# Kernel tuning notes

Measured on AMD Instinct MI355X. Metric: run time of the kernel, lower is better.

The kernel has to match this reference:

```python
import jax, jax.numpy as jnp
import numpy as np

N = 100000      # total nodes (batched graphs)
E = 1200000     # total edges
A = 256         # annotation size (hidden_size_orig)
H = 64          # gnn_h_size
T = 4           # num_edge_types
STEPS = 6       # num_timesteps
B = 64          # number of graphs in the batch
NUM_CLS = 2


def setup_inputs() -> dict:
    key = jax.random.key(0)
    ks = jax.random.split(key, 16)
    annotation = jax.random.normal(ks[0], (N, A), dtype=jnp.float32)
    src = jax.random.randint(ks[1], (E,), 0, N, dtype=jnp.int32)
    dst = jax.random.randint(ks[2], (E,), 0, N, dtype=jnp.int32)
    etypes = jax.random.randint(ks[3], (E,), 0, T, dtype=jnp.int32)
    graph_ids = jnp.sort(jax.random.randint(ks[4], (N,), 0, B, dtype=jnp.int32))

    def lin(k, fan_in, shape):
        return jax.random.normal(k, shape, dtype=jnp.float32) / np.sqrt(fan_in).astype(np.float32)

    params = {
        'reduce_W': lin(ks[5], A, (A, H)),
        'reduce_b': jnp.zeros((H,), jnp.float32),
        'edge_W': lin(ks[6], H, (T, H, H)),      # per-edge-type linear
        'edge_b': jnp.zeros((T, H), jnp.float32),
        'gru_Wi': lin(ks[7], H, (3 * H, H)),     # torch GRUCell layout: r,z,n
        'gru_bi': jnp.zeros((3 * H,), jnp.float32),
        'gru_Wh': lin(ks[8], H, (3 * H, H)),
        'gru_bh': jnp.zeros((3 * H,), jnp.float32),
        'gate_W': lin(ks[9], 2 * H, (2 * H, 1)),
        'gate_b': jnp.zeros((1,), jnp.float32),
        'out_W': lin(ks[10], 2 * H, (2 * H, NUM_CLS)),
        'out_b': jnp.zeros((NUM_CLS,), jnp.float32),
    }
    return dict(annotation=annotation, src=src, dst=dst, etypes=etypes,
                graph_ids=graph_ids, **params)


def reference(annotation, src, dst, etypes, graph_ids,
              reduce_W, reduce_b, edge_W, edge_b,
              gru_Wi, gru_bi, gru_Wh, gru_bh,
              gate_W, gate_b, out_W, out_b):
    # reduce_layer
    h0 = annotation @ reduce_W + reduce_b            # [N, H]

    def step(h, _):
        # per-edge-type linear on all nodes: [T, N, H]
        transformed = jnp.einsum('nh,thk->tnk', h, edge_W) + edge_b[:, None, :]
        msg = transformed[etypes, src]               # [E, H] gather per edge
        a = jax.ops.segment_sum(msg, dst, num_segments=N)  # scatter-add
        # GRUCell(a, h)
        gi = a @ gru_Wi.T + gru_bi
        gh = h @ gru_Wh.T + gru_bh
        i_r, i_z, i_n = jnp.split(gi, 3, axis=-1)
        h_r, h_z, h_n = jnp.split(gh, 3, axis=-1)
        r = jax.nn.sigmoid(i_r + h_r)
        z = jax.nn.sigmoid(i_z + h_z)
        n = jnp.tanh(i_n + r * h_n)
        h_new = (1.0 - z) * n + z * h
        return h_new, None

    h, _ = jax.lax.scan(step, h0, None, length=STEPS)

    feat = jnp.concatenate([h, h0], axis=-1)         # [N, 2H]

    # GlobalAttentionPooling: segment softmax over gate scores, weighted sum
    gate = feat @ gate_W + gate_b                    # [N, 1]
    gmax = jax.ops.segment_max(gate, graph_ids, num_segments=B)
    gmax = jnp.where(jnp.isfinite(gmax), gmax, 0.0)  # guard empty graphs
    e = jnp.exp(gate - gmax[graph_ids])
    denom = jax.ops.segment_sum(e, graph_ids, num_segments=B)
    alpha = e / denom[graph_ids]                     # [N, 1]
    readout = jax.ops.segment_sum(alpha * feat, graph_ids, num_segments=B)  # [B, 2H]

    logits = readout @ out_W + out_b                 # [B, 2]
    return logits
```

## Files before the change

kernel.cpp:

```cpp
#include <hip/hip_runtime.h>
#include <cstdint>
#include <cstddef>

#define N_NODES 100000
#define N_EDGES 1200000
#define ASIZE 256
#define HSIZE 64
#define NTYPES 4
#define NSTEPS 6
#define NGRAPH 64
#define PS 16

static __device__ __forceinline__ float sigmoidf_(float x) { return 1.0f / (1.0f + expf(-x)); }

__global__ void k_count(const int* __restrict__ dst, int* __restrict__ deg) {
    int e = blockIdx.x * 256 + threadIdx.x;
    if (e < N_EDGES) atomicAdd(&deg[dst[e]], 1);
}

__global__ void k_scan1(const int* __restrict__ deg, int* __restrict__ rs, int* __restrict__ part) {
    __shared__ int sh[256];
    int t = threadIdx.x;
    int base = blockIdx.x * 1024 + t * 4;
    int v0 = (base + 0 < N_NODES) ? deg[base + 0] : 0;
    int v1 = (base + 1 < N_NODES) ? deg[base + 1] : 0;
    int v2 = (base + 2 < N_NODES) ? deg[base + 2] : 0;
    int v3 = (base + 3 < N_NODES) ? deg[base + 3] : 0;
    int s = v0 + v1 + v2 + v3;
    sh[t] = s;
    __syncthreads();
    for (int off = 1; off < 256; off <<= 1) {
        int x = (t >= off) ? sh[t - off] : 0;
        __syncthreads();
        sh[t] += x;
        __syncthreads();
    }
    int excl = sh[t] - s;
    if (t == 255) part[blockIdx.x] = sh[255];
    if (base + 0 < N_NODES) rs[base + 0] = excl;
    if (base + 1 < N_NODES) rs[base + 1] = excl + v0;
    if (base + 2 < N_NODES) rs[base + 2] = excl + v0 + v1;
    if (base + 3 < N_NODES) rs[base + 3] = excl + v0 + v1 + v2;
}

__global__ void k_scan2(int* __restrict__ part, int* __restrict__ rs, int nb) {
    if (threadIdx.x == 0 && blockIdx.x == 0) {
        int run = 0;
        for (int i = 0; i < nb; ++i) { int v = part[i]; part[i] = run; run += v; }
        rs[N_NODES] = run;
    }
}

__global__ void k_scan3(int* __restrict__ rs, const int* __restrict__ part) {
    int i = blockIdx.x * 256 + threadIdx.x;
    if (i < N_NODES) rs[i] += part[i >> 10];
}

__global__ void k_fill(const int* __restrict__ src, const int* __restrict__ dst,
                       const int* __restrict__ ety, const int* __restrict__ rs,
                       int* __restrict__ cur, int* __restrict__ colidx) {
    int e = blockIdx.x * 256 + threadIdx.x;
    if (e < N_EDGES) {
        int d = dst[e];
        int pos = rs[d] + atomicAdd(&cur[d], 1);
        colidx[pos] = src[e] * 448 + 192 + ety[e] * 64;
    }
}

__global__ void k_prep2(const float* __restrict__ Wh, const float* __restrict__ Bh,
                        const float* __restrict__ eW, const float* __restrict__ eb,
                        const float* __restrict__ Wi, const float* __restrict__ Bi,
                        float* __restrict__ W448, float* __restrict__ bias448,
                        float* __restrict__ WiA, float* __restrict__ biA) {
    int idx = blockIdx.x * 256 + threadIdx.x;
    if (idx < 64 * 448) {
        int k = idx / 448, m = idx % 448;
        float v;
        if (m < 192) {
            int j = m / 3, g = m % 3;
            v = Wh[(g * 64 + j) * 64 + k];
        } else {
            v = eW[(size_t)(m - 192 >> 6) * 4096 + k * 64 + ((m - 192) & 63)];
        }
        W448[idx] = v;
    }
    if (idx < 64 * 192) {
        int k = idx / 192, m = idx % 192;
        int j = m / 3, g = m % 3;
        WiA[idx] = Wi[(g * 64 + j) * 64 + k];
    }
    if (idx < 448) {
        bias448[idx] = (idx < 192) ? Bh[(idx % 3) * 64 + idx / 3] : eb[idx - 192];
    }
    if (idx < 192) {
        biA[idx] = Bi[(idx % 3) * 64 + idx / 3];
    }
}

__global__ __launch_bounds__(256) void k_gemm(const float* __restrict__ X, int ldx, int K,
                                              const float* __restrict__ W, int ldw,
                                              const float* __restrict__ bias,
                                              float* __restrict__ Y, float* __restrict__ Y2,
                                              int M) {
    __shared__ float sX[128 * 66];
    __shared__ float sW[64 * 64];
    int tid = threadIdx.x;
    int mtile = blockIdx.x * 64;
    int ntile = blockIdx.y * 128;
    int tc4 = (tid & 15) * 4;
    int tr = tid >> 4;
    float4 acc[8];
#pragma unroll
    for (int i = 0; i < 8; ++i) acc[i] = make_float4(0.f, 0.f, 0.f, 0.f);

    int nkc = K >> 6;
    for (int kc = 0; kc < nkc; ++kc) {
        if (kc) __syncthreads();
#pragma unroll
        for (int i = 0; i < 8; ++i) {
            int lin4 = (i * 256 + tid) * 4;
            int nl = lin4 >> 6, kk = lin4 & 63;
            int n = ntile + nl;
            float4 v = make_float4(0.f, 0.f, 0.f, 0.f);
            if (n < N_NODES) v = *(const float4*)(X + (size_t)n * ldx + kc * 64 + kk);
            float* d = sX + nl * 66 + kk;
            d[0] = v.x; d[1] = v.y; d[2] = v.z; d[3] = v.w;
        }
#pragma unroll
        for (int i = 0; i < 4; ++i) {
            int lin4 = (i * 256 + tid) * 4;
            int kk = lin4 >> 6, c = lin4 & 63;
            float4 v = *(const float4*)(W + (size_t)(kc * 64 + kk) * ldw + mtile + c);
            *(float4*)(sW + kk * 64 + c) = v;
        }
        __syncthreads();
        const float* xr = sX + tr * 8 * 66;
        const float* wr = sW + tc4;
        for (int kk = 0; kk < 64; kk += 2) {
            float4 wA = *(const float4*)(wr + kk * 64);
            float4 wB = *(const float4*)(wr + (kk + 1) * 64);
            float xA[8], xB[8];
#pragma unroll
            for (int i = 0; i < 8; ++i) { xA[i] = xr[i * 66 + kk]; xB[i] = xr[i * 66 + kk + 1]; }
#pragma unroll
            for (int i = 0; i < 8; ++i) {
                acc[i].x = fmaf(xA[i], wA.x, acc[i].x);
                acc[i].y = fmaf(xA[i], wA.y, acc[i].y);
                acc[i].z = fmaf(xA[i], wA.z, acc[i].z);
                acc[i].w = fmaf(xA[i], wA.w, acc[i].w);
            }
#pragma unroll
            for (int i = 0; i < 8; ++i) {
                acc[i].x = fmaf(xB[i], wB.x, acc[i].x);
                acc[i].y = fmaf(xB[i], wB.y, acc[i].y);
                acc[i].z = fmaf(xB[i], wB.z, acc[i].z);
                acc[i].w = fmaf(xB[i], wB.w, acc[i].w);
            }
        }
    }
    float4 bv = *(const float4*)(bias + mtile + tc4);
#pragma unroll
    for (int i = 0; i < 8; ++i) {
        int n = ntile + tr * 8 + i;
        if (n < N_NODES) {
            float4 y;
            y.x = acc[i].x + bv.x; y.y = acc[i].y + bv.y;
            y.z = acc[i].z + bv.z; y.w = acc[i].w + bv.w;
            *(float4*)(Y + (size_t)n * M + mtile + tc4) = y;
            if (Y2) *(float4*)(Y2 + (size_t)n * M + mtile + tc4) = y;
        }
    }
}

__global__ void k_aggregate(const float* __restrict__ buf1, const int* __restrict__ rs,
                            const int* __restrict__ colidx, float* __restrict__ a) {
    int l = threadIdx.x & 63;
    int n = blockIdx.x * 4 + (threadIdx.x >> 6);
    int beg = rs[n], end = rs[n + 1];
    float a0 = 0.f, a1 = 0.f, a2 = 0.f, a3 = 0.f;
    int s = beg;
    for (; s + 3 < end; s += 4) {
        int c0 = colidx[s], c1 = colidx[s + 1], c2 = colidx[s + 2], c3 = colidx[s + 3];
        a0 += buf1[(size_t)c0 + l];
        a1 += buf1[(size_t)c1 + l];
        a2 += buf1[(size_t)c2 + l];
        a3 += buf1[(size_t)c3 + l];
    }
    for (; s < end; ++s) a0 += buf1[(size_t)colidx[s] + l];
    a[(size_t)n * 64 + l] = (a0 + a1) + (a2 + a3);
}

__global__ __launch_bounds__(256) void k_gruF(const float* __restrict__ A,
                                              const float* __restrict__ WiA,
                                              const float* __restrict__ biA,
                                              const float* __restrict__ buf1,
                                              float* __restrict__ H) {
    __shared__ float sX[64 * 34];
    __shared__ float sW[32 * 192];
    int tid = threadIdx.x;
    int ntile = blockIdx.x * 64;
    int tc = tid & 15;
    int tr = tid >> 4;
    float acc[4][12];
#pragma unroll
    for (int i = 0; i < 4; ++i)
#pragma unroll
        for (int c = 0; c < 12; ++c) acc[i][c] = 0.f;

    for (int kc = 0; kc < 2; ++kc) {
        if (kc) __syncthreads();
#pragma unroll
        for (int i = 0; i < 2; ++i) {
            int lin4 = (i * 256 + tid) * 4;
            int nl = lin4 >> 5, kk = lin4 & 31;
            int n = ntile + nl;
            float4 v = make_float4(0.f, 0.f, 0.f, 0.f);
            if (n < N_NODES) v = *(const float4*)(A + (size_t)n * 64 + kc * 32 + kk);
            float* d = sX + nl * 34 + kk;
            d[0] = v.x; d[1] = v.y; d[2] = v.z; d[3] = v.w;
        }
        {
            int kk = tid >> 3, c = (tid & 7) * 24;
            const float* srcp = WiA + (size_t)(kc * 32 + kk) * 192 + c;
            float* d = sW + kk * 192 + c;
#pragma unroll
            for (int u = 0; u < 6; ++u) *(float4*)(d + 4 * u) = *(const float4*)(srcp + 4 * u);
        }
        __syncthreads();
        const float* xr = sX + tr * 4 * 34;
        const float* wr = sW + tc * 12;
        for (int kk = 0; kk < 32; kk += 2) {
            float4 w0 = *(const float4*)(wr + kk * 192);
            float4 w1 = *(const float4*)(wr + kk * 192 + 4);
            float4 w2 = *(const float4*)(wr + kk * 192 + 8);
            float4 u0 = *(const float4*)(wr + (kk + 1) * 192);
            float4 u1 = *(const float4*)(wr + (kk + 1) * 192 + 4);
            float4 u2 = *(const float4*)(wr + (kk + 1) * 192 + 8);
            float xA[4], xB[4];
#pragma unroll
            for (int i = 0; i < 4; ++i) { xA[i] = xr[i * 34 + kk]; xB[i] = xr[i * 34 + kk + 1]; }
#pragma unroll
            for (int i = 0; i < 4; ++i) {
                acc[i][0]  = fmaf(xA[i], w0.x, acc[i][0]);
                acc[i][1]  = fmaf(xA[i], w0.y, acc[i][1]);
                acc[i][2]  = fmaf(xA[i], w0.z, acc[i][2]);
                acc[i][3]  = fmaf(xA[i], w0.w, acc[i][3]);
                acc[i][4]  = fmaf(xA[i], w1.x, acc[i][4]);
                acc[i][5]  = fmaf(xA[i], w1.y, acc[i][5]);
                acc[i][6]  = fmaf(xA[i], w1.z, acc[i][6]);
                acc[i][7]  = fmaf(xA[i], w1.w, acc[i][7]);
                acc[i][8]  = fmaf(xA[i], w2.x, acc[i][8]);
                acc[i][9]  = fmaf(xA[i], w2.y, acc[i][9]);
                acc[i][10] = fmaf(xA[i], w2.z, acc[i][10]);
                acc[i][11] = fmaf(xA[i], w2.w, acc[i][11]);
            }
#pragma unroll
            for (int i = 0; i < 4; ++i) {
                acc[i][0]  = fmaf(xB[i], u0.x, acc[i][0]);
                acc[i][1]  = fmaf(xB[i], u0.y, acc[i][1]);
                acc[i][2]  = fmaf(xB[i], u0.z, acc[i][2]);
                acc[i][3]  = fmaf(xB[i], u0.w, acc[i][3]);
                acc[i][4]  = fmaf(xB[i], u1.x, acc[i][4]);
                acc[i][5]  = fmaf(xB[i], u1.y, acc[i][5]);
                acc[i][6]  = fmaf(xB[i], u1.z, acc[i][6]);
                acc[i][7]  = fmaf(xB[i], u1.w, acc[i][7]);
                acc[i][8]  = fmaf(xB[i], u2.x, acc[i][8]);
                acc[i][9]  = fmaf(xB[i], u2.y, acc[i][9]);
                acc[i][10] = fmaf(xB[i], u2.z, acc[i][10]);
                acc[i][11] = fmaf(xB[i], u2.w, acc[i][11]);
            }
        }
    }
    float bb[12];
    {
        float4 b0 = *(const float4*)(biA + tc * 12);
        float4 b1 = *(const float4*)(biA + tc * 12 + 4);
        float4 b2 = *(const float4*)(biA + tc * 12 + 8);
        bb[0] = b0.x; bb[1] = b0.y; bb[2] = b0.z; bb[3] = b0.w;
        bb[4] = b1.x; bb[5] = b1.y; bb[6] = b1.z; bb[7] = b1.w;
        bb[8] = b2.x; bb[9] = b2.y; bb[10] = b2.z; bb[11] = b2.w;
    }
#pragma unroll
    for (int i = 0; i < 4; ++i) {
        int n = ntile + tr * 4 + i;
        if (n >= N_NODES) continue;
        const float* ghp = buf1 + (size_t)n * 448 + tc * 12;
        float gg[12];
        float4 g0 = *(const float4*)(ghp);
        float4 g1 = *(const float4*)(ghp + 4);
        float4 g2 = *(const float4*)(ghp + 8);
        gg[0] = g0.x; gg[1] = g0.y; gg[2] = g0.z; gg[3] = g0.w;
        gg[4] = g1.x; gg[5] = g1.y; gg[6] = g1.z; gg[7] = g1.w;
        gg[8] = g2.x; gg[9] = g2.y; gg[10] = g2.z; gg[11] = g2.w;
        float4 hv = *(const float4*)(H + (size_t)n * 64 + tc * 4);
        float res[4];
#pragma unroll
        for (int jj = 0; jj < 4; ++jj) {
            int c = jj * 3;
            float r = sigmoidf_(acc[i][c] + bb[c] + gg[c]);
            float z = sigmoidf_(acc[i][c + 1] + bb[c + 1] + gg[c + 1]);
            float nn = tanhf(acc[i][c + 2] + bb[c + 2] + r * gg[c + 2]);
            float hj = (jj == 0) ? hv.x : (jj == 1) ? hv.y : (jj == 2) ? hv.z : hv.w;
            res[jj] = (1.f - z) * nn + z * hj;
        }
        float4 o; o.x = res[0]; o.y = res[1]; o.z = res[2]; o.w = res[3];
        *(float4*)(H + (size_t)n * 64 + tc * 4) = o;
    }
}

__global__ void k_bounds(const int* __restrict__ gid, int* __restrict__ start) {
    int n = blockIdx.x * 256 + threadIdx.x;
    if (n < N_NODES) {
        int g = gid[n];
        if (n == 0) {
            for (int x = 0; x <= g; ++x) start[x] = 0;
        } else {
            int pg = gid[n - 1];
            for (int x = pg + 1; x <= g; ++x) start[x] = n;
        }
        if (n == N_NODES - 1) {
            for (int x = g + 1; x <= NGRAPH; ++x) start[x] = N_NODES;
        }
    }
}

__global__ void k_gate2(const float* __restrict__ H, const float* __restrict__ H0,
                        const float* __restrict__ gW, const float* __restrict__ gb,
                        float* __restrict__ gate) {
    int l = threadIdx.x & 63;
    int n = blockIdx.x * 4 + (threadIdx.x >> 6);
    float v = H[(size_t)n * 64 + l] * gW[l] + H0[(size_t)n * 64 + l] * gW[64 + l];
    for (int off = 32; off > 0; off >>= 1) v += __shfl_xor(v, off, 64);
    if (l == 0) gate[n] = v + gb[0];
}

__global__ __launch_bounds__(64) void k_poolA(const float* __restrict__ gate,
                                              const int* __restrict__ start,
                                              float* __restrict__ pmax) {
    int g = blockIdx.x, s = blockIdx.y;
    int beg = start[g], len = start[g + 1] - beg;
    int sb = beg + (int)((long long)len * s / PS);
    int se = beg + (int)((long long)len * (s + 1) / PS);
    float m = -INFINITY;
    for (int n = sb + threadIdx.x; n < se; n += 64) m = fmaxf(m, gate[n]);
    for (int off = 32; off > 0; off >>= 1) m = fmaxf(m, __shfl_xor(m, off, 64));
    if (threadIdx.x == 0) pmax[g * PS + s] = m;
}

__global__ void k_poolB(const float* __restrict__ pmax, float* __restrict__ gm) {
    int g = threadIdx.x;
    float m = -INFINITY;
    for (int s = 0; s < PS; ++s) m = fmaxf(m, pmax[g * PS + s]);
    if (!isfinite(m)) m = 0.0f;
    gm[g] = m;
}

__global__ __launch_bounds__(256) void k_poolC(const float* __restrict__ H,
                                               const float* __restrict__ H0,
                                               const float* __restrict__ gate,
                                               const int* __restrict__ start,
                                               const float* __restrict__ gm,
                                               float* __restrict__ pnum,
                                               float* __restrict__ pden) {
    int g = blockIdx.x, s = blockIdx.y;
    int beg = start[g], len = start[g + 1] - beg;
    int sb = beg + (int)((long long)len * s / PS);
    int se = beg + (int)((long long)len * (s + 1) / PS);
    int t = threadIdx.x;
    int lane = t & 63, wave = t >> 6;
    float m = gm[g];
    __shared__ float shh[4][64], sh0[4][64], ses[4];
    float ah = 0.f, ah0 = 0.f, es = 0.f;
    for (int n = sb + wave; n < se; n += 4) {
        float e = expf(gate[n] - m);
        es += e;
        ah  += e * H [(size_t)n * 64 + lane];
        ah0 += e * H0[(size_t)n * 64 + lane];
    }
    shh[wave][lane] = ah; sh0[wave][lane] = ah0;
    if (lane == 0) ses[wave] = es;
    __syncthreads();
    if (wave == 0) {
        float r  = shh[0][lane] + shh[1][lane] + shh[2][lane] + shh[3][lane];
        float r0 = sh0[0][lane] + sh0[1][lane] + sh0[2][lane] + sh0[3][lane];
        int base = (g * PS + s) * 128;
        pnum[base + lane]      = r;
        pnum[base + 64 + lane] = r0;
        if (lane == 0) pden[g * PS + s] = ses[0] + ses[1] + ses[2] + ses[3];
    }
}

__global__ __launch_bounds__(128) void k_poolD(const float* __restrict__ pnum,
                                               const float* __restrict__ pden,
                                               float* __restrict__ ro) {
    int g = blockIdx.x;
    int c = threadIdx.x;
    float den = 0.f;
    for (int s = 0; s < PS; ++s) den += pden[g * PS + s];
    float nu = 0.f;
    for (int s = 0; s < PS; ++s) nu += pnum[(g * PS + s) * 128 + c];
    ro[g * 128 + c] = (den > 0.f) ? nu / den : 0.f;
}

__global__ void k_logits(const float* __restrict__ ro, const float* __restrict__ oW,
                         const float* __restrict__ ob, float* __restrict__ out) {
    int t = threadIdx.x;
    int b = t >> 1;
    int c = t & 1;
    float acc = ob[c];
    for (int k = 0; k < 128; ++k) acc = fmaf(ro[b * 128 + k], oW[k * 2 + c], acc);
    out[b * 2 + c] = acc;
}

extern "C" void kernel_launch(void* const* d_in, const int* in_sizes, int n_in,
                              void* d_out, int out_size, void* d_ws, size_t ws_size,
                              hipStream_t stream) {
    (void)in_sizes; (void)n_in; (void)out_size; (void)ws_size;
    const float* ann = (const float*)d_in[0];
    const int* src   = (const int*)d_in[1];
    const int* dst   = (const int*)d_in[2];
    const int* ety   = (const int*)d_in[3];
    const int* gid   = (const int*)d_in[4];
    const float* rW  = (const float*)d_in[5];
    const float* rb  = (const float*)d_in[6];
    const float* eW  = (const float*)d_in[7];
    const float* eb  = (const float*)d_in[8];
    const float* Wi  = (const float*)d_in[9];
    const float* Bi  = (const float*)d_in[10];
    const float* Wh  = (const float*)d_in[11];
    const float* Bh  = (const float*)d_in[12];
    const float* gW  = (const float*)d_in[13];
    const float* gb  = (const float*)d_in[14];
    const float* oW  = (const float*)d_in[15];
    const float* ob  = (const float*)d_in[16];
    float* out = (float*)d_out;

    char* p = (char*)d_ws;
    auto take = [&](size_t nbytes) -> void* {
        void* r = (void*)p;
        p += (nbytes + 255) & ~((size_t)255);
        return r;
    };
    float* h0      = (float*)take((size_t)N_NODES * 64 * 4);
    float* h       = (float*)take((size_t)N_NODES * 64 * 4);
    float* abuf    = (float*)take((size_t)N_NODES * 64 * 4);
    float* buf1    = (float*)take((size_t)N_NODES * 448 * 4);
    float* W448    = (float*)take(64 * 448 * 4);
    float* bias448 = (float*)take(448 * 4);
    float* WiA     = (float*)take(64 * 192 * 4);
    float* biA     = (float*)take(192 * 4);
    int* deg       = (int*)take((size_t)N_NODES * 4);
    int* cur       = (int*)take((size_t)N_NODES * 4);
    int* rs        = (int*)take((size_t)(N_NODES + 1) * 4);
    int* part      = (int*)take(512);
    int* colidx    = (int*)take((size_t)N_EDGES * 4);
    float* gate    = (float*)take((size_t)N_NODES * 4);
    int* start     = (int*)take((size_t)(NGRAPH + 1) * 4);
    float* pmax    = (float*)take(NGRAPH * PS * 4);
    float* gm      = (float*)take(NGRAPH * 4);
    float* pnum    = (float*)take((size_t)NGRAPH * PS * 128 * 4);
    float* pden    = (float*)take(NGRAPH * PS * 4);
    float* ro      = (float*)take(NGRAPH * 128 * 4);

    hipMemsetAsync(deg, 0, (size_t)N_NODES * 4, stream);
    hipMemsetAsync(cur, 0, (size_t)N_NODES * 4, stream);
    k_count<<<(N_EDGES + 255) / 256, 256, 0, stream>>>(dst, deg);
    int nb = (N_NODES + 1023) / 1024;
    k_scan1<<<nb, 256, 0, stream>>>(deg, rs, part);
    k_scan2<<<1, 64, 0, stream>>>(part, rs, nb);
    k_scan3<<<(N_NODES + 255) / 256, 256, 0, stream>>>(rs, part);
    k_fill<<<(N_EDGES + 255) / 256, 256, 0, stream>>>(src, dst, ety, rs, cur, colidx);

    k_prep2<<<112, 256, 0, stream>>>(Wh, Bh, eW, eb, Wi, Bi, W448, bias448, WiA, biA);
    k_bounds<<<(N_NODES + 255) / 256, 256, 0, stream>>>(gid, start);

    int ntiles = (N_NODES + 127) / 128;

    k_gemm<<<dim3(1, ntiles), 256, 0, stream>>>(ann, ASIZE, ASIZE, rW, 64, rb, h, h0, 64);

    for (int s = 0; s < NSTEPS; ++s) {
        k_gemm<<<dim3(7, ntiles), 256, 0, stream>>>(h, 64, 64, W448, 448, bias448,
                                                    buf1, nullptr, 448);
        k_aggregate<<<N_NODES / 4, 256, 0, stream>>>(buf1, rs, colidx, abuf);
        k_gruF<<<(N_NODES + 63) / 64, 256, 0, stream>>>(abuf, WiA, biA, buf1, h);
    }

    k_gate2<<<N_NODES / 4, 256, 0, stream>>>(h, h0, gW, gb, gate);
    k_poolA<<<dim3(NGRAPH, PS), 64, 0, stream>>>(gate, start, pmax);
    k_poolB<<<1, 64, 0, stream>>>(pmax, gm);
    k_poolC<<<dim3(NGRAPH, PS), 256, 0, stream>>>(h, h0, gate, start, gm, pnum, pden);
    k_poolD<<<NGRAPH, 128, 0, stream>>>(pnum, pden, ro);
    k_logits<<<1, 128, 0, stream>>>(ro, oW, ob, out);
}
```

Before: 1.588 ms.

## Specialize GEMMs: reuse X tile across all output columns, prefetch weights

```diff
diff --git a/kernel.cpp b/kernel.cpp
--- a/kernel.cpp
+++ b/kernel.cpp
@@ -97,48 +97,52 @@
     }
 }
 
-__global__ __launch_bounds__(256) void k_gemm(const float* __restrict__ X, int ldx, int K,
-                                              const float* __restrict__ W, int ldw,
-                                              const float* __restrict__ bias,
-                                              float* __restrict__ Y, float* __restrict__ Y2,
-                                              int M) {
+__global__ __launch_bounds__(256) void k_gemm_step(const float* __restrict__ X,
+                                                   const float* __restrict__ W,
+                                                   const float* __restrict__ bias,
+                                                   float* __restrict__ Y) {
     __shared__ float sX[128 * 66];
     __shared__ float sW[64 * 64];
     int tid = threadIdx.x;
-    int mtile = blockIdx.x * 64;
-    int ntile = blockIdx.y * 128;
+    int ntile = blockIdx.x * 128;
     int tc4 = (tid & 15) * 4;
     int tr = tid >> 4;
-    float4 acc[8];
-#pragma unroll
-    for (int i = 0; i < 8; ++i) acc[i] = make_float4(0.f, 0.f, 0.f, 0.f);
-
-    int nkc = K >> 6;
-    for (int kc = 0; kc < nkc; ++kc) {
-        if (kc) __syncthreads();
-#pragma unroll
-        for (int i = 0; i < 8; ++i) {
-            int lin4 = (i * 256 + tid) * 4;
-            int nl = lin4 >> 6, kk = lin4 & 63;
-            int n = ntile + nl;
-            float4 v = make_float4(0.f, 0.f, 0.f, 0.f);
-            if (n < N_NODES) v = *(const float4*)(X + (size_t)n * ldx + kc * 64 + kk);
-            float* d = sX + nl * 66 + kk;
-            d[0] = v.x; d[1] = v.y; d[2] = v.z; d[3] = v.w;
-        }
-#pragma unroll
-        for (int i = 0; i < 4; ++i) {
-            int lin4 = (i * 256 + tid) * 4;
-            int kk = lin4 >> 6, c = lin4 & 63;
-            float4 v = *(const float4*)(W + (size_t)(kc * 64 + kk) * ldw + mtile + c);
-            *(float4*)(sW + kk * 64 + c) = v;
-        }
-        __syncthreads();
-        const float* xr = sX + tr * 8 * 66;
-        const float* wr = sW + tc4;
+    int swr = tid >> 4;
+    int swc = (tid & 15) * 4;
+
+#pragma unroll
+    for (int i = 0; i < 8; ++i) {
+        int lin4 = (i * 256 + tid) * 4;
+        int nl = lin4 >> 6, kk = lin4 & 63;
+        int n = ntile + nl;
+        float4 v = make_float4(0.f, 0.f, 0.f, 0.f);
+        if (n < N_NODES) v = *(const float4*)(X + (size_t)n * 64 + kk);
+        float* d = sX + nl * 66 + kk;
+        d[0] = v.x; d[1] = v.y; d[2] = v.z; d[3] = v.w;
+    }
+    float4 wreg[4];
+#pragma unroll
+    for (int i = 0; i < 4; ++i)
+        wreg[i] = *(const float4*)(W + (size_t)(i * 16 + swr) * 448 + swc);
+#pragma unroll
+    for (int i = 0; i < 4; ++i)
+        *(float4*)(sW + (i * 16 + swr) * 64 + swc) = wreg[i];
+    __syncthreads();
+
+    const float* xr = sX + tr * 8 * 66;
+    const float* wrp = sW + tc4;
+    for (int m = 0; m < 7; ++m) {
+        if (m < 6) {
+#pragma unroll
+            for (int i = 0; i < 4; ++i)
+                wreg[i] = *(const float4*)(W + (size_t)(i * 16 + swr) * 448 + (m + 1) * 64 + swc);
+        }
+        float4 acc[8];
+#pragma unroll
+        for (int i = 0; i < 8; ++i) acc[i] = make_float4(0.f, 0.f, 0.f, 0.f);
         for (int kk = 0; kk < 64; kk += 2) {
-            float4 wA = *(const float4*)(wr + kk * 64);
-            float4 wB = *(const float4*)(wr + (kk + 1) * 64);
+            float4 wA = *(const float4*)(wrp + kk * 64);
+            float4 wB = *(const float4*)(wrp + (kk + 1) * 64);
             float xA[8], xB[8];
 #pragma unroll
             for (int i = 0; i < 8; ++i) { xA[i] = xr[i * 66 + kk]; xB[i] = xr[i * 66 + kk + 1]; }
@@ -157,8 +161,112 @@
                 acc[i].w = fmaf(xB[i], wB.w, acc[i].w);
             }
         }
-    }
-    float4 bv = *(const float4*)(bias + mtile + tc4);
+        float4 bv = *(const float4*)(bias + m * 64 + tc4);
+        if (m < 6) {
+            __syncthreads();
+#pragma unroll
+            for (int i = 0; i < 4; ++i)
+                *(float4*)(sW + (i * 16 + swr) * 64 + swc) = wreg[i];
+            __syncthreads();
+        }
+#pragma unroll
+        for (int i = 0; i < 8; ++i) {
+            int n = ntile + tr * 8 + i;
+            if (n < N_NODES) {
+                float4 y;
+                y.x = acc[i].x + bv.x; y.y = acc[i].y + bv.y;
+                y.z = acc[i].z + bv.z; y.w = acc[i].w + bv.w;
+                *(float4*)(Y + (size_t)n * 448 + m * 64 + tc4) = y;
+            }
+        }
+    }
+}
+
+__global__ __launch_bounds__(256) void k_gemm_red(const float* __restrict__ X,
+                                                  const float* __restrict__ W,
+                                                  const float* __restrict__ bias,
+                                                  float* __restrict__ Y,
+                                                  float* __restrict__ Y2) {
+    __shared__ float sX[128 * 66];
+    __shared__ float sW[64 * 64];
+    int tid = threadIdx.x;
+    int ntile = blockIdx.x * 128;
+    int tc4 = (tid & 15) * 4;
+    int tr = tid >> 4;
+    int swr = tid >> 4;
+    int swc = (tid & 15) * 4;
+
+    float4 acc[8];
+#pragma unroll
+    for (int i = 0; i < 8; ++i) acc[i] = make_float4(0.f, 0.f, 0.f, 0.f);
+
+    float4 xreg[8];
+    float4 wreg[4];
+#pragma unroll
+    for (int i = 0; i < 8; ++i) {
+        int lin4 = (i * 256 + tid) * 4;
+        int nl = lin4 >> 6, kk = lin4 & 63;
+        int n = ntile + nl;
+        float4 v = make_float4(0.f, 0.f, 0.f, 0.f);
+        if (n < N_NODES) v = *(const float4*)(X + (size_t)n * 256 + kk);
+        xreg[i] = v;
+    }
+#pragma unroll
+    for (int i = 0; i < 4; ++i)
+        wreg[i] = *(const float4*)(W + (size_t)(i * 16 + swr) * 64 + swc);
+
+    for (int kc = 0; kc < 4; ++kc) {
+#pragma unroll
+        for (int i = 0; i < 8; ++i) {
+            int lin4 = (i * 256 + tid) * 4;
+            int nl = lin4 >> 6, kk = lin4 & 63;
+            float* d = sX + nl * 66 + kk;
+            d[0] = xreg[i].x; d[1] = xreg[i].y; d[2] = xreg[i].z; d[3] = xreg[i].w;
+        }
+#pragma unroll
+        for (int i = 0; i < 4; ++i)
+            *(float4*)(sW + (i * 16 + swr) * 64 + swc) = wreg[i];
+        __syncthreads();
+        if (kc < 3) {
+#pragma unroll
+            for (int i = 0; i < 8; ++i) {
+                int lin4 = (i * 256 + tid) * 4;
+                int nl = lin4 >> 6, kk = lin4 & 63;
+                int n = ntile + nl;
+                float4 v = make_float4(0.f, 0.f, 0.f, 0.f);
+                if (n < N_NODES) v = *(const float4*)(X + (size_t)n * 256 + (kc + 1) * 64 + kk);
+                xreg[i] = v;
+            }
+#pragma unroll
+            for (int i = 0; i < 4; ++i)
+                wreg[i] = *(const float4*)(W + (size_t)((kc + 1) * 64 + i * 16 + swr) * 64 + swc);
+        }
+        const float* xr = sX + tr * 8 * 66;
+        const float* wrp = sW + tc4;
+        for (int kk = 0; kk < 64; kk += 2) {
+            float4 wA = *(const float4*)(wrp + kk * 64);
+            float4 wB = *(const float4*)(wrp + (kk + 1) * 64);
+            float xA[8], xB[8];
+#pragma unroll
+            for (int i = 0; i < 8; ++i) { xA[i] = xr[i * 66 + kk]; xB[i] = xr[i * 66 + kk + 1]; }
+#pragma unroll
+            for (int i = 0; i < 8; ++i) {
+                acc[i].x = fmaf(xA[i], wA.x, acc[i].x);
+                acc[i].y = fmaf(xA[i], wA.y, acc[i].y);
+                acc[i].z = fmaf(xA[i], wA.z, acc[i].z);
+                acc[i].w = fmaf(xA[i], wA.w, acc[i].w);
+            }
+#pragma unroll
+            for (int i = 0; i < 8; ++i) {
+                acc[i].x = fmaf(xB[i], wB.x, acc[i].x);
+                acc[i].y = fmaf(xB[i], wB.y, acc[i].y);
+                acc[i].z = fmaf(xB[i], wB.z, acc[i].z);
+                acc[i].w = fmaf(xB[i], wB.w, acc[i].w);
+            }
+        }
+        if (kc < 3) __syncthreads();
+    }
+    float4 bv = *(const float4*)(bias + tc4);
 #pragma unroll
     for (int i = 0; i < 8; ++i) {
         int n = ntile + tr * 8 + i;
@@ -166,8 +274,8 @@
             float4 y;
             y.x = acc[i].x + bv.x; y.y = acc[i].y + bv.y;
             y.z = acc[i].z + bv.z; y.w = acc[i].w + bv.w;
-            *(float4*)(Y + (size_t)n * M + mtile + tc4) = y;
-            if (Y2) *(float4*)(Y2 + (size_t)n * M + mtile + tc4) = y;
+            *(float4*)(Y + (size_t)n * 64 + tc4) = y;
+            *(float4*)(Y2 + (size_t)n * 64 + tc4) = y;
         }
     }
 }
@@ -476,11 +584,10 @@
 
     int ntiles = (N_NODES + 127) / 128;
 
-    k_gemm<<<dim3(1, ntiles), 256, 0, stream>>>(ann, ASIZE, ASIZE, rW, 64, rb, h, h0, 64);
+    k_gemm_red<<<ntiles, 256, 0, stream>>>(ann, rW, rb, h, h0);
 
     for (int s = 0; s < NSTEPS; ++s) {
-        k_gemm<<<dim3(7, ntiles), 256, 0, stream>>>(h, 64, 64, W448, 448, bias448,
-                                                    buf1, nullptr, 448);
+        k_gemm_step<<<ntiles, 256, 0, stream>>>(h, W448, bias448, buf1);
         k_aggregate<<<N_NODES / 4, 256, 0, stream>>>(buf1, rs, colidx, abuf);
         k_gruF<<<(N_NODES + 63) / 64, 256, 0, stream>>>(abuf, WiA, biA, buf1, h);
     }
```

New measurement: 1.721 ms. 1.08x slower.
